# Performance work log

Measured on AMD Instinct MI355X. Metric: run time of the kernel, lower is better.

## Reference

```python
import jax, jax.numpy as jnp
import numpy as np
from jax import lax

DILATIONS = (1, 3, 9, 9, 3, 1)  # six mid blocks after the 1x1 input conv


def bilinear_sample(fm, verts):
    # fm: [B,H,W,C]; verts: [B,N,2] in [-1,1]; axis 0 of verts maps to H, axis 1 to W.
    # Matches jax.scipy.ndimage.map_coordinates(order=1, mode='constant'):
    # each out-of-bounds corner contributes 0.
    B, H, W, C = fm.shape
    scale = jnp.array([H - 1, W - 1], fm.dtype) / 2.0
    coords = (verts + 1.0) * scale  # [B,N,2]
    vy, vx = coords[..., 0], coords[..., 1]
    y0 = jnp.floor(vy)
    x0 = jnp.floor(vx)
    wy = (vy - y0)[..., None]
    wx = (vx - x0)[..., None]
    y0i = y0.astype(jnp.int32)
    x0i = x0.astype(jnp.int32)
    fm_flat = fm.reshape(B, H * W, C)

    def corner(yi, xi):
        valid = (yi >= 0) & (yi < H) & (xi >= 0) & (xi < W)
        idx = jnp.clip(yi, 0, H - 1) * W + jnp.clip(xi, 0, W - 1)  # [B,N]
        vals = jnp.take_along_axis(fm_flat, idx[..., None], axis=1)  # [B,N,C]
        return jnp.where(valid[..., None], vals, jnp.zeros((), fm.dtype))

    return ((1 - wy) * (1 - wx) * corner(y0i, x0i)
            + (1 - wy) * wx * corner(y0i, x0i + 1)
            + wy * (1 - wx) * corner(y0i + 1, x0i)
            + wy * wx * corner(y0i + 1, x0i + 1))


def conv1d(x, w, b, dil):
    # x: [B,N,Cin], w: [K,Cin,Cout]; flax nnx.Conv default: stride 1, SAME padding.
    out = lax.conv_general_dilated(x, w, (1,), 'SAME', rhs_dilation=(dil,),
                                   dimension_numbers=('NWC', 'WIO', 'NWC'))
    return out if b is None else out + b


def setup_inputs() -> dict:
    key = jax.random.key(0)
    ks = jax.random.split(key, 8)
    B, N, H, W, Cf, Ch = 16, 1024, 256, 256, 126, 512
    D = Cf + 2
    vertices = jax.random.uniform(ks[0], (B, N, 2), jnp.float32, -1.0, 1.0)
    feature_map = jax.random.normal(ks[1], (B, H, W, Cf), jnp.float32)
    w0 = jax.random.normal(ks[2], (1, D, Ch), jnp.float32) / np.float32(np.sqrt(D))
    b0 = jnp.zeros((Ch,), jnp.float32)
    ws = jax.random.normal(ks[3], (6, 3, Ch, Ch), jnp.float32) / np.float32(np.sqrt(3 * Ch))
    bs = jnp.zeros((6, Ch), jnp.float32)
    w_off = jax.random.normal(ks[4], (1, Ch, 2), jnp.float32) / np.float32(np.sqrt(Ch))
    return {"vertices": vertices, "feature_map": feature_map,
            "w0": w0, "b0": b0, "ws": ws, "bs": bs, "w_off": w_off}


def reference(vertices, feature_map, w0, b0, ws, bs, w_off):
    feat = bilinear_sample(feature_map, vertices)          # [B,N,Cf]
    x = jnp.concatenate([feat, vertices], axis=-1)         # [B,N,Cf+2]
    x = jax.nn.relu(conv1d(x, w0, b0, 1))                  # 1x1 input conv
    for i, dil in enumerate(DILATIONS):                    # fixed 6-layer stack
        x = jax.nn.relu(conv1d(x, ws[i], bs[i], dil))
    return conv1d(x, w_off, None, 1)                       # [B,N,2] offsets
```

## Files before the change

### kernel.cpp

```cpp
#include <hip/hip_runtime.h>

typedef __attribute__((ext_vector_type(4))) float f32x4;
typedef __attribute__((ext_vector_type(8))) _Float16 f16x8;

#define BM 128
#define BK 64

#define OFF_W0T 0
#define OFF_WT  131072
#define OFF_X0  (OFF_WT + 6*512*1536*2)
#define OFF_Y0  (OFF_X0 + 16384*128*2)
#define OFF_Y1  (OFF_Y0 + 16*1056*512*2)

__device__ __forceinline__ void load_lds16(const void* g, void* s) {
    __builtin_amdgcn_global_load_lds(
        (const __attribute__((address_space(1))) void*)g,
        (__attribute__((address_space(3))) void*)s, 16, 0, 0);
}

__global__ __launch_bounds__(256)
void wprep(const float* __restrict__ ws, const float* __restrict__ w0,
           _Float16* __restrict__ wt, _Float16* __restrict__ w0t)
{
    __shared__ float t[64][65];
    const int tid = threadIdx.x;
    const int tr = tid >> 6;
    const int tc = tid & 63;
    const int z = blockIdx.z;
    if (z < 18) {
        const int l = z / 3, tp = z % 3;
        const float* src = ws + (size_t)z * 512 * 512;
        const int ci0 = blockIdx.y * 64, co0 = blockIdx.x * 64;
        #pragma unroll
        for (int i = 0; i < 16; ++i) { int r = i*4 + tr; t[r][tc] = src[(ci0 + r)*512 + co0 + tc]; }
        __syncthreads();
        _Float16* dst = wt + (size_t)l * 512 * 1536;
        #pragma unroll
        for (int i = 0; i < 16; ++i) { int r = i*4 + tr; dst[(co0 + r)*1536 + tp*512 + ci0 + tc] = (_Float16)t[tc][r]; }
    } else {
        if (blockIdx.y >= 2) return;
        const int ci0 = blockIdx.y * 64, co0 = blockIdx.x * 64;
        #pragma unroll
        for (int i = 0; i < 16; ++i) { int r = i*4 + tr; t[r][tc] = w0[(ci0 + r)*512 + co0 + tc]; }
        __syncthreads();
        #pragma unroll
        for (int i = 0; i < 16; ++i) { int r = i*4 + tr; w0t[(co0 + r)*128 + ci0 + tc] = (_Float16)t[tc][r]; }
    }
}

__global__ __launch_bounds__(256)
void zeropad(_Float16* __restrict__ Y0, _Float16* __restrict__ Y1)
{
    const int i = blockIdx.x * 256 + threadIdx.x;
    const unsigned c2   = i & 255;
    const unsigned t2   = ((unsigned)i) >> 8;
    const unsigned prow = t2 & 31;
    const unsigned b    = (t2 >> 5) & 15;
    const unsigned buf  = t2 >> 9;
    const unsigned row  = prow < 16 ? prow : (1024 + prow);
    unsigned* p = (unsigned*)(buf ? Y1 : Y0);
    p[((size_t)b * 1056 + row) * 256 + c2] = 0u;
}

__global__ __launch_bounds__(256)
void sample_kernel(const float* __restrict__ verts, const float* __restrict__ fm,
                   _Float16* __restrict__ X0)
{
    const int p = blockIdx.x * 4 + (threadIdx.x >> 6);
    const int lane = threadIdx.x & 63;
    const int b = p >> 10;
    const float vy = verts[p*2], vx = verts[p*2 + 1];
    const float cy = (vy + 1.f) * 127.5f;
    const float cx = (vx + 1.f) * 127.5f;
    const float fy = floorf(cy), fx = floorf(cx);
    const int y0 = (int)fy, x0 = (int)fx;
    const float wy = cy - fy, wx = cx - fx;
    float w00 = (1.f - wy) * (1.f - wx), w01 = (1.f - wy) * wx;
    float w10 = wy * (1.f - wx),         w11 = wy * wx;
    const bool vy0 = (unsigned)y0 < 256u, vy1 = (unsigned)(y0 + 1) < 256u;
    const bool vx0 = (unsigned)x0 < 256u, vx1 = (unsigned)(x0 + 1) < 256u;
    w00 = (vy0 && vx0) ? w00 : 0.f;
    w01 = (vy0 && vx1) ? w01 : 0.f;
    w10 = (vy1 && vx0) ? w10 : 0.f;
    w11 = (vy1 && vx1) ? w11 : 0.f;
    const int yc0 = min(max(y0, 0), 255), yc1 = min(max(y0 + 1, 0), 255);
    const int xc0 = min(max(x0, 0), 255), xc1 = min(max(x0 + 1, 0), 255);
    const float* base = fm + (size_t)b * (256 * 256 * 126);
    const float* p00 = base + (yc0 * 256 + xc0) * 126;
    const float* p01 = base + (yc0 * 256 + xc1) * 126;
    const float* p10 = base + (yc1 * 256 + xc0) * 126;
    const float* p11 = base + (yc1 * 256 + xc1) * 126;
    _Float16* xr = X0 + (size_t)p * 128;
    for (int c = lane; c < 126; c += 64) {
        float a = w00 * p00[c] + w01 * p01[c] + w10 * p10[c] + w11 * p11[c];
        xr[c] = (_Float16)a;
    }
    if (lane < 2) xr[126 + lane] = (_Float16)(lane ? vx : vy);
}

template<int KTOT>
__global__ __launch_bounds__(256)
void conv_gemm(const _Float16* __restrict__ A, int a_row_stride, int a_batch_stride,
               const _Float16* __restrict__ WT, const float* __restrict__ bias,
               _Float16* __restrict__ Out, int o_row_stride, int o_batch_stride,
               int dil)
{
    __shared__ _Float16 Ald[BM * BK];
    __shared__ _Float16 Bld[BM * BK];
    const int tid  = threadIdx.x;
    const int wid  = tid >> 6;
    const int lane = tid & 63;
    const int b    = blockIdx.x >> 3;
    const int n0   = (blockIdx.x & 7) * BM;
    const int co0  = blockIdx.y * BM;
    const int wm   = wid >> 1, wn = wid & 1;

    const _Float16* Ab = A + (size_t)b * a_batch_stride + (size_t)n0 * a_row_stride;

    f32x4 acc[4][4] = {};

    const int srow = lane >> 3;
    const int scol = (lane & 7) * 8;

    for (int ks = 0; ks < KTOT / BK; ++ks) {
        int ci0, shift;
        if (KTOT == 128) { ci0 = ks * 64; shift = 0; }
        else             { int t = ks >> 3; ci0 = (ks & 7) * 64; shift = (t - 1) * dil; }
        const _Float16* Arow = Ab + (long)shift * a_row_stride + ci0 + scol;
        const _Float16* Brow = WT + (size_t)co0 * KTOT + ks * 64 + scol;
        #pragma unroll
        for (int i = 0; i < 4; ++i) {
            const int r0 = wid * 32 + i * 8;
            load_lds16(Arow + (size_t)(r0 + srow) * a_row_stride, &Ald[r0 * BK]);
            load_lds16(Brow + (size_t)(r0 + srow) * KTOT,         &Bld[r0 * BK]);
        }
        __syncthreads();
        #pragma unroll
        for (int kf = 0; kf < 2; ++kf) {
            f16x8 af[4], bfr[4];
            #pragma unroll
            for (int f = 0; f < 4; ++f) {
                af[f]  = *(const f16x8*)&Ald[(wm*64 + f*16 + (lane & 15)) * BK + kf*32 + (lane >> 4) * 8];
                bfr[f] = *(const f16x8*)&Bld[(wn*64 + f*16 + (lane & 15)) * BK + kf*32 + (lane >> 4) * 8];
            }
            #pragma unroll
            for (int m = 0; m < 4; ++m)
                #pragma unroll
                for (int n = 0; n < 4; ++n)
                    acc[m][n] = __builtin_amdgcn_mfma_f32_16x16x32_f16(af[m], bfr[n], acc[m][n], 0, 0, 0);
        }
        __syncthreads();
    }

    _Float16* Ob = Out + (size_t)b * o_batch_stride + (size_t)n0 * o_row_stride;
    #pragma unroll
    for (int n = 0; n < 4; ++n) {
        const int co = co0 + wn*64 + n*16 + (lane & 15);
        const float bv = bias[co];
        #pragma unroll
        for (int m = 0; m < 4; ++m) {
            #pragma unroll
            for (int j = 0; j < 4; ++j) {
                const int row = wm*64 + m*16 + (lane >> 4)*4 + j;
                float v = acc[m][n][j] + bv;
                v = fmaxf(v, 0.f);
                Ob[(size_t)row * o_row_stride + co] = (_Float16)v;
            }
        }
    }
}

#define NT8 24
__global__ __launch_bounds__(512, 2)
void conv_gemm8(const _Float16* __restrict__ A, const _Float16* __restrict__ WT,
                const float* __restrict__ bias, _Float16* __restrict__ Out, int dil)
{
    extern __shared__ _Float16 smem[];
    _Float16* Ald = smem;
    _Float16* Bld = smem + 3 * 256 * 64;

    const int tid  = threadIdx.x;
    const int wid  = tid >> 6;
    const int lane = tid & 63;
    const int wm   = wid >> 1;
    const int wn   = wid & 1;

    const int orig = blockIdx.x;
    const int swz  = (orig & 7) * 32 + (orig >> 3);
    const int nblk = swz & 3;
    const int mblk = swz >> 2;
    const int b     = mblk >> 2;
    const int n0row = (mblk & 3) * 256;
    const int co0   = nblk * 128;

    const _Float16* Ab = A + (size_t)b * (1056 * 512) + (size_t)n0row * 512;

    const int srow = lane >> 3;
    const int scol = (((lane & 7) ^ (lane >> 3)) << 3);

    f32x4 acc[4][4] = {};

    auto stageA = [&](int kt, int c, int ci0, int shift) {
        const int grow = 64 * c + 8 * wid + srow;
        const _Float16* src = Ab + (long)(grow + shift) * 512 + ci0 + scol;
        _Float16* dst = Ald + (kt % 3) * (256 * 64) + (64 * c + 8 * wid) * 64;
        load_lds16(src, dst);
    };
    auto stageB = [&](int kt, int c, int kk) {
        const int grow = 64 * c + 8 * wid + srow;
        const _Float16* src = WT + (size_t)(co0 + grow) * 1536 + kk + scol;
        _Float16* dst = Bld + (kt % 3) * (128 * 64) + (64 * c + 8 * wid) * 64;
        load_lds16(src, dst);
    };
    auto kinfo = [&](int ks, int& ci0, int& shift) {
        const int t = ks >> 3; ci0 = (ks & 7) * 64; shift = (t - 1) * dil;
    };

    {
        int ci0, sh;
        kinfo(0, ci0, sh);
        stageA(0, 0, ci0, sh); stageA(0, 1, ci0, sh); stageA(0, 2, ci0, sh); stageA(0, 3, ci0, sh);
        stageB(0, 0, 0); stageB(0, 1, 0);
        kinfo(1, ci0, sh);
        stageA(1, 0, ci0, sh); stageA(1, 1, ci0, sh); stageA(1, 2, ci0, sh); stageA(1, 3, ci0, sh);
        stageB(1, 0, 64); stageB(1, 1, 64);
    }

    #pragma unroll 1
    for (int kt = 0; kt < NT8; ++kt) {
        __builtin_amdgcn_sched_barrier(0);
        if (kt < NT8 - 1) asm volatile("s_waitcnt vmcnt(6)" ::: "memory");
        else              asm volatile("s_waitcnt vmcnt(0)" ::: "memory");
        __builtin_amdgcn_s_barrier();
        __builtin_amdgcn_sched_barrier(0);

        const _Float16* Abuf = Ald + (kt % 3) * (256 * 64);
        const _Float16* Bbuf = Bld + (kt % 3) * (128 * 64);
        const bool do_stage = (kt + 2 < NT8);
        int nci0 = 0, nsh = 0;
        if (do_stage) kinfo(kt + 2, nci0, nsh);

        f16x8 bfr[4][2], af[4][2];
        #pragma unroll
        for (int nf = 0; nf < 4; ++nf) {
            const int row = wn * 64 + nf * 16 + (lane & 15);
            #pragma unroll
            for (int kf = 0; kf < 2; ++kf) {
                const int slot = (kf * 4 + (lane >> 4)) ^ (row & 7);
                bfr[nf][kf] = *(const f16x8*)&Bbuf[row * 64 + slot * 8];
            }
        }
        {
            const int row = wm * 64 + 0 * 16 + (lane & 15);
            #pragma unroll
            for (int kf = 0; kf < 2; ++kf) {
                const int slot = (kf * 4 + (lane >> 4)) ^ (row & 7);
                af[0][kf] = *(const f16x8*)&Abuf[row * 64 + slot * 8];
            }
        }
        #pragma unroll
        for (int nf = 0; nf < 4; ++nf)
            #pragma unroll
            for (int kf = 0; kf < 2; ++kf)
                acc[0][nf] = __builtin_amdgcn_mfma_f32_16x16x32_f16(af[0][kf], bfr[nf][kf], acc[0][nf], 0, 0, 0);
        {
            const int row = wm * 64 + 1 * 16 + (lane & 15);
            #pragma unroll
            for (int kf = 0; kf < 2; ++kf) {
                const int slot = (kf * 4 + (lane >> 4)) ^ (row & 7);
                af[1][kf] = *(const f16x8*)&Abuf[row * 64 + slot * 8];
            }
        }
        if (do_stage) { stageA(kt + 2, 0, nci0, nsh); stageA(kt + 2, 1, nci0, nsh); stageA(kt + 2, 2, nci0, nsh); }
        #pragma unroll
        for (int nf = 0; nf < 4; ++nf)
            #pragma unroll
            for (int kf = 0; kf < 2; ++kf)
                acc[1][nf] = __builtin_amdgcn_mfma_f32_16x16x32_f16(af[1][kf], bfr[nf][kf], acc[1][nf], 0, 0, 0);
        {
            const int row = wm * 64 + 2 * 16 + (lane & 15);
            #pragma unroll
            for (int kf = 0; kf < 2; ++kf) {
                const int slot = (kf * 4 + (lane >> 4)) ^ (row & 7);
                af[2][kf] = *(const f16x8*)&Abuf[row * 64 + slot * 8];
            }
        }
        if (do_stage) { stageA(kt + 2, 3, nci0, nsh); stageB(kt + 2, 0, (kt + 2) * 64); stageB(kt + 2, 1, (kt + 2) * 64); }
        #pragma unroll
        for (int nf = 0; nf < 4; ++nf)
            #pragma unroll
            for (int kf = 0; kf < 2; ++kf)
                acc[2][nf] = __builtin_amdgcn_mfma_f32_16x16x32_f16(af[2][kf], bfr[nf][kf], acc[2][nf], 0, 0, 0);
        {
            const int row = wm * 64 + 3 * 16 + (lane & 15);
            #pragma unroll
            for (int kf = 0; kf < 2; ++kf) {
                const int slot = (kf * 4 + (lane >> 4)) ^ (row & 7);
                af[3][kf] = *(const f16x8*)&Abuf[row * 64 + slot * 8];
            }
        }
        #pragma unroll
        for (int nf = 0; nf < 4; ++nf)
            #pragma unroll
            for (int kf = 0; kf < 2; ++kf)
                acc[3][nf] = __builtin_amdgcn_mfma_f32_16x16x32_f16(af[3][kf], bfr[nf][kf], acc[3][nf], 0, 0, 0);

        __builtin_amdgcn_sched_group_barrier(0x100, 10, 0);
        __builtin_amdgcn_sched_group_barrier(0x008,  8, 0);
        __builtin_amdgcn_sched_group_barrier(0x100,  2, 0);
        __builtin_amdgcn_sched_group_barrier(0x070,  3, 0);
        __builtin_amdgcn_sched_group_barrier(0x008,  8, 0);
        __builtin_amdgcn_sched_group_barrier(0x100,  2, 0);
        __builtin_amdgcn_sched_group_barrier(0x070,  3, 0);
        __builtin_amdgcn_sched_group_barrier(0x008,  8, 0);
        __builtin_amdgcn_sched_group_barrier(0x100,  2, 0);
        __builtin_amdgcn_sched_group_barrier(0x008,  8, 0);
    }

    _Float16* Ob = Out + (size_t)b * (1056 * 512) + (size_t)n0row * 512;
    #pragma unroll
    for (int nf = 0; nf < 4; ++nf) {
        const int co = co0 + wn * 64 + nf * 16 + (lane & 15);
        const float bv = bias[co];
        #pragma unroll
        for (int m = 0; m < 4; ++m) {
            #pragma unroll
            for (int j = 0; j < 4; ++j) {
                const int row = wm * 64 + m * 16 + (lane >> 4) * 4 + j;
                float v = acc[m][nf][j] + bv;
                v = fmaxf(v, 0.f);
                Ob[(size_t)row * 512 + co] = (_Float16)v;
            }
        }
    }
}

__global__ __launch_bounds__(256)
void final_conv(const _Float16* __restrict__ Y, const float* __restrict__ woff,
                float* __restrict__ out)
{
    const int r = blockIdx.x * 4 + (threadIdx.x >> 6);
    const int lane = threadIdx.x & 63;
    const int b = r >> 10, n = r & 1023;
    const _Float16* yp = Y + ((size_t)b * 1056 + n) * 512 + lane * 8;
    f16x8 yv = *(const f16x8*)yp;
    const int ci0 = lane * 8;
    float s0 = 0.f, s1 = 0.f;
    #pragma unroll
    for (int e = 0; e < 8; ++e) {
        float y = (float)yv[e];
        s0 += y * woff[(ci0 + e) * 2 + 0];
        s1 += y * woff[(ci0 + e) * 2 + 1];
    }
    #pragma unroll
    for (int off = 32; off; off >>= 1) {
        s0 += __shfl_down(s0, off);
        s1 += __shfl_down(s1, off);
    }
    if (lane == 0) { out[r*2] = s0; out[r*2 + 1] = s1; }
}

extern "C" void kernel_launch(void* const* d_in, const int* in_sizes, int n_in,
                              void* d_out, int out_size, void* d_ws, size_t ws_size,
                              hipStream_t stream)
{
    const float* verts = (const float*)d_in[0];
    const float* fm    = (const float*)d_in[1];
    const float* w0    = (const float*)d_in[2];
    const float* b0    = (const float*)d_in[3];
    const float* ws    = (const float*)d_in[4];
    const float* bs    = (const float*)d_in[5];
    const float* woff  = (const float*)d_in[6];
    float* out = (float*)d_out;

    char* wsp = (char*)d_ws;
    _Float16* W0T = (_Float16*)(wsp + OFF_W0T);
    _Float16* WT  = (_Float16*)(wsp + OFF_WT);
    _Float16* X0  = (_Float16*)(wsp + OFF_X0);
    _Float16* Y0  = (_Float16*)(wsp + OFF_Y0);
    _Float16* Y1  = (_Float16*)(wsp + OFF_Y1);
    _Float16* Y0i = Y0 + 16 * 512;
    _Float16* Y1i = Y1 + 16 * 512;

    hipFuncSetAttribute(reinterpret_cast<const void*>(&conv_gemm8),
                        hipFuncAttributeMaxDynamicSharedMemorySize, 147456);

    wprep<<<dim3(8, 8, 19), 256, 0, stream>>>(ws, w0, WT, W0T);
    zeropad<<<1024, 256, 0, stream>>>(Y0, Y1);
    sample_kernel<<<4096, 256, 0, stream>>>(verts, fm, X0);

    conv_gemm<128><<<dim3(128, 4), 256, 0, stream>>>(
        X0, 128, 1024 * 128, W0T, b0, Y0i, 512, 1056 * 512, 1);

    const int DIL[6] = {1, 3, 9, 9, 3, 1};
    _Float16* bufs[2] = {Y0i, Y1i};
    for (int l = 0; l < 6; ++l) {
        conv_gemm8<<<256, 512, 147456, stream>>>(
            bufs[l & 1],
            WT + (size_t)l * 512 * 1536, bs + (size_t)l * 512,
            bufs[(l + 1) & 1], DIL[l]);
    }

    final_conv<<<4096, 256, 0, stream>>>(bufs[0], woff, out);
}
```

Baseline: 198.4 us.

## Reuse one A tile across all three conv taps with shifted LDS reads

The dilated-conv GEMM now stages a 320-row A chunk per 64-channel slice once and reads it three times with tap-dependent row shifts, instead of reloading a fresh 256-row A tile for every (tap, channel) k-step. The k-loop is restructured around channel chunks with compile-time tap specialisation, a double-buffered A halo tile, and three B buffers, each with its own wait counts and schedule groups. This cuts global and L2 traffic for A by roughly a factor of three and lowers dynamic LDS to 128 KB. In exchange the wait logic is more intricate and the swizzle key now depends on the shifted row, which risks bank conflicts or races if the counts are off. The halo assumes dil ≤ 32.

```diff
diff --git a/kernel.cpp b/kernel.cpp
--- a/kernel.cpp
+++ b/kernel.cpp
@@ -17,6 +17,8 @@
         (const __attribute__((address_space(1))) void*)g,
         (__attribute__((address_space(3))) void*)s, 16, 0, 0);
 }
+
+template<int N> struct IC { static constexpr int v = N; };
 
 __global__ __launch_bounds__(256)
 void wprep(const float* __restrict__ ws, const float* __restrict__ w0,
@@ -170,14 +172,15 @@
     }
 }
 
-#define NT8 24
+#define ACH_ELEMS (320 * 64)
+#define BBUF_ELEMS (128 * 64)
 __global__ __launch_bounds__(512, 2)
 void conv_gemm8(const _Float16* __restrict__ A, const _Float16* __restrict__ WT,
                 const float* __restrict__ bias, _Float16* __restrict__ Out, int dil)
 {
     extern __shared__ _Float16 smem[];
     _Float16* Ald = smem;
-    _Float16* Bld = smem + 3 * 256 * 64;
+    _Float16* Bld = smem + 2 * ACH_ELEMS;
 
     const int tid  = threadIdx.x;
     const int wid  = tid >> 6;
@@ -200,45 +203,38 @@
 
     f32x4 acc[4][4] = {};
 
-    auto stageA = [&](int kt, int c, int ci0, int shift) {
-        const int grow = 64 * c + 8 * wid + srow;
-        const _Float16* src = Ab + (long)(grow + shift) * 512 + ci0 + scol;
-        _Float16* dst = Ald + (kt % 3) * (256 * 64) + (64 * c + 8 * wid) * 64;
-        load_lds16(src, dst);
+    auto stageA1 = [&](int cn, int i) {
+        const int rb = 8 * (wid + 8 * i);
+        const _Float16* src = Ab + (long)(rb + srow - 32) * 512 + cn * 64 + scol;
+        load_lds16(src, Ald + (cn & 1) * ACH_ELEMS + rb * 64);
     };
-    auto stageB = [&](int kt, int c, int kk) {
-        const int grow = 64 * c + 8 * wid + srow;
-        const _Float16* src = WT + (size_t)(co0 + grow) * 1536 + kk + scol;
-        _Float16* dst = Bld + (kt % 3) * (128 * 64) + (64 * c + 8 * wid) * 64;
-        load_lds16(src, dst);
+    auto stageB1 = [&](int c2, int t2, int cc) {
+        const int grow = 64 * cc + 8 * wid + srow;
+        const _Float16* src = WT + (size_t)(co0 + grow) * 1536 + (t2 * 512 + c2 * 64) + scol;
+        load_lds16(src, Bld + t2 * BBUF_ELEMS + (64 * cc + 8 * wid) * 64);
     };
-    auto kinfo = [&](int ks, int& ci0, int& shift) {
-        const int t = ks >> 3; ci0 = (ks & 7) * 64; shift = (t - 1) * dil;
-    };
-
-    {
-        int ci0, sh;
-        kinfo(0, ci0, sh);
-        stageA(0, 0, ci0, sh); stageA(0, 1, ci0, sh); stageA(0, 2, ci0, sh); stageA(0, 3, ci0, sh);
-        stageB(0, 0, 0); stageB(0, 1, 0);
-        kinfo(1, ci0, sh);
-        stageA(1, 0, ci0, sh); stageA(1, 1, ci0, sh); stageA(1, 2, ci0, sh); stageA(1, 3, ci0, sh);
-        stageB(1, 0, 64); stageB(1, 1, 64);
-    }
-
-    #pragma unroll 1
-    for (int kt = 0; kt < NT8; ++kt) {
+
+    stageA1(0, 0); stageA1(0, 1); stageA1(0, 2); stageA1(0, 3); stageA1(0, 4);
+    stageB1(0, 0, 0); stageB1(0, 0, 1);
+    stageB1(0, 1, 0); stageB1(0, 1, 1);
+
+    auto body = [&](auto TAPc, auto DOAc, int c) {
+        constexpr int TAP = decltype(TAPc)::v;
+        constexpr int DOA = decltype(DOAc)::v;
+
         __builtin_amdgcn_sched_barrier(0);
-        if (kt < NT8 - 1) asm volatile("s_waitcnt vmcnt(6)" ::: "memory");
-        else              asm volatile("s_waitcnt vmcnt(0)" ::: "memory");
+        if constexpr (TAP == 1 && DOA)       asm volatile("s_waitcnt vmcnt(7)" ::: "memory");
+        else if constexpr (TAP == 2 && !DOA) asm volatile("s_waitcnt vmcnt(0)" ::: "memory");
+        else                                 asm volatile("s_waitcnt vmcnt(2)" ::: "memory");
         __builtin_amdgcn_s_barrier();
         __builtin_amdgcn_sched_barrier(0);
 
-        const _Float16* Abuf = Ald + (kt % 3) * (256 * 64);
-        const _Float16* Bbuf = Bld + (kt % 3) * (128 * 64);
-        const bool do_stage = (kt + 2 < NT8);
-        int nci0 = 0, nsh = 0;
-        if (do_stage) kinfo(kt + 2, nci0, nsh);
+        const _Float16* Abuf = Ald + (c & 1) * ACH_ELEMS;
+        const _Float16* Bbuf = Bld + TAP * BBUF_ELEMS;
+        const int shift = (TAP - 1) * dil;
+        const int rbase = 32 + wm * 64 + (lane & 15) + shift;
+        const int akey  = rbase & 7;
+        const int bkey  = lane & 7;
 
         f16x8 bfr[4][2], af[4][2];
         #pragma unroll
@@ -246,58 +242,61 @@
             const int row = wn * 64 + nf * 16 + (lane & 15);
             #pragma unroll
             for (int kf = 0; kf < 2; ++kf) {
-                const int slot = (kf * 4 + (lane >> 4)) ^ (row & 7);
+                const int slot = (kf * 4 + (lane >> 4)) ^ bkey;
                 bfr[nf][kf] = *(const f16x8*)&Bbuf[row * 64 + slot * 8];
             }
         }
-        {
-            const int row = wm * 64 + 0 * 16 + (lane & 15);
-            #pragma unroll
-            for (int kf = 0; kf < 2; ++kf) {
-                const int slot = (kf * 4 + (lane >> 4)) ^ (row & 7);
-                af[0][kf] = *(const f16x8*)&Abuf[row * 64 + slot * 8];
-            }
+        #pragma unroll
+        for (int kf = 0; kf < 2; ++kf) {
+            const int slot = (kf * 4 + (lane >> 4)) ^ akey;
+            af[0][kf] = *(const f16x8*)&Abuf[rbase * 64 + slot * 8];
         }
         #pragma unroll
         for (int nf = 0; nf < 4; ++nf)
             #pragma unroll
             for (int kf = 0; kf < 2; ++kf)
                 acc[0][nf] = __builtin_amdgcn_mfma_f32_16x16x32_f16(af[0][kf], bfr[nf][kf], acc[0][nf], 0, 0, 0);
-        {
-            const int row = wm * 64 + 1 * 16 + (lane & 15);
-            #pragma unroll
-            for (int kf = 0; kf < 2; ++kf) {
-                const int slot = (kf * 4 + (lane >> 4)) ^ (row & 7);
-                af[1][kf] = *(const f16x8*)&Abuf[row * 64 + slot * 8];
-            }
-        }
-        if (do_stage) { stageA(kt + 2, 0, nci0, nsh); stageA(kt + 2, 1, nci0, nsh); stageA(kt + 2, 2, nci0, nsh); }
+        #pragma unroll
+        for (int kf = 0; kf < 2; ++kf) {
+            const int slot = (kf * 4 + (lane >> 4)) ^ akey;
+            af[1][kf] = *(const f16x8*)&Abuf[(rbase + 16) * 64 + slot * 8];
+        }
+        if constexpr (TAP == 0 && DOA) {
+            stageA1(c + 1, 0); stageA1(c + 1, 1); stageA1(c + 1, 2); stageA1(c + 1, 3);
+        } else if constexpr (TAP == 0) {
+            stageB1(7, 2, 0);
+        } else if constexpr (DOA) {
+            if constexpr (TAP == 1) stageB1(c + 1, 0, 0);
+            else                    stageB1(c + 1, 1, 0);
+        }
         #pragma unroll
         for (int nf = 0; nf < 4; ++nf)
             #pragma unroll
             for (int kf = 0; kf < 2; ++kf)
                 acc[1][nf] = __builtin_amdgcn_mfma_f32_16x16x32_f16(af[1][kf], bfr[nf][kf], acc[1][nf], 0, 0, 0);
-        {
-            const int row = wm * 64 + 2 * 16 + (lane & 15);
-            #pragma unroll
-            for (int kf = 0; kf < 2; ++kf) {
-                const int slot = (kf * 4 + (lane >> 4)) ^ (row & 7);
-                af[2][kf] = *(const f16x8*)&Abuf[row * 64 + slot * 8];
-            }
-        }
-        if (do_stage) { stageA(kt + 2, 3, nci0, nsh); stageB(kt + 2, 0, (kt + 2) * 64); stageB(kt + 2, 1, (kt + 2) * 64); }
+        #pragma unroll
+        for (int kf = 0; kf < 2; ++kf) {
+            const int slot = (kf * 4 + (lane >> 4)) ^ akey;
+            af[2][kf] = *(const f16x8*)&Abuf[(rbase + 32) * 64 + slot * 8];
+        }
+        if constexpr (TAP == 0 && DOA) {
+            stageA1(c + 1, 4);
+            stageB1(c, 2, 0); stageB1(c, 2, 1);
+        } else if constexpr (TAP == 0) {
+            stageB1(7, 2, 1);
+        } else if constexpr (DOA) {
+            if constexpr (TAP == 1) stageB1(c + 1, 0, 1);
+            else                    stageB1(c + 1, 1, 1);
+        }
         #pragma unroll
         for (int nf = 0; nf < 4; ++nf)
             #pragma unroll
             for (int kf = 0; kf < 2; ++kf)
                 acc[2][nf] = __builtin_amdgcn_mfma_f32_16x16x32_f16(af[2][kf], bfr[nf][kf], acc[2][nf], 0, 0, 0);
-        {
-            const int row = wm * 64 + 3 * 16 + (lane & 15);
-            #pragma unroll
-            for (int kf = 0; kf < 2; ++kf) {
-                const int slot = (kf * 4 + (lane >> 4)) ^ (row & 7);
-                af[3][kf] = *(const f16x8*)&Abuf[row * 64 + slot * 8];
-            }
+        #pragma unroll
+        for (int kf = 0; kf < 2; ++kf) {
+            const int slot = (kf * 4 + (lane >> 4)) ^ akey;
+            af[3][kf] = *(const f16x8*)&Abuf[(rbase + 48) * 64 + slot * 8];
         }
         #pragma unroll
         for (int nf = 0; nf < 4; ++nf)
@@ -305,17 +304,42 @@
             for (int kf = 0; kf < 2; ++kf)
                 acc[3][nf] = __builtin_amdgcn_mfma_f32_16x16x32_f16(af[3][kf], bfr[nf][kf], acc[3][nf], 0, 0, 0);
 
-        __builtin_amdgcn_sched_group_barrier(0x100, 10, 0);
-        __builtin_amdgcn_sched_group_barrier(0x008,  8, 0);
-        __builtin_amdgcn_sched_group_barrier(0x100,  2, 0);
-        __builtin_amdgcn_sched_group_barrier(0x070,  3, 0);
-        __builtin_amdgcn_sched_group_barrier(0x008,  8, 0);
-        __builtin_amdgcn_sched_group_barrier(0x100,  2, 0);
-        __builtin_amdgcn_sched_group_barrier(0x070,  3, 0);
-        __builtin_amdgcn_sched_group_barrier(0x008,  8, 0);
-        __builtin_amdgcn_sched_group_barrier(0x100,  2, 0);
-        __builtin_amdgcn_sched_group_barrier(0x008,  8, 0);
-    }
+        if constexpr (DOA) {
+            if constexpr (TAP == 0) {
+                __builtin_amdgcn_sched_group_barrier(0x100, 10, 0);
+                __builtin_amdgcn_sched_group_barrier(0x008,  8, 0);
+                __builtin_amdgcn_sched_group_barrier(0x100,  2, 0);
+                __builtin_amdgcn_sched_group_barrier(0x070,  4, 0);
+                __builtin_amdgcn_sched_group_barrier(0x008,  8, 0);
+                __builtin_amdgcn_sched_group_barrier(0x100,  2, 0);
+                __builtin_amdgcn_sched_group_barrier(0x070,  3, 0);
+                __builtin_amdgcn_sched_group_barrier(0x008,  8, 0);
+                __builtin_amdgcn_sched_group_barrier(0x100,  2, 0);
+                __builtin_amdgcn_sched_group_barrier(0x008,  8, 0);
+            } else {
+                __builtin_amdgcn_sched_group_barrier(0x100, 10, 0);
+                __builtin_amdgcn_sched_group_barrier(0x008,  8, 0);
+                __builtin_amdgcn_sched_group_barrier(0x100,  2, 0);
+                __builtin_amdgcn_sched_group_barrier(0x070,  1, 0);
+                __builtin_amdgcn_sched_group_barrier(0x008,  8, 0);
+                __builtin_amdgcn_sched_group_barrier(0x100,  2, 0);
+                __builtin_amdgcn_sched_group_barrier(0x070,  1, 0);
+                __builtin_amdgcn_sched_group_barrier(0x008,  8, 0);
+                __builtin_amdgcn_sched_group_barrier(0x100,  2, 0);
+                __builtin_amdgcn_sched_group_barrier(0x008,  8, 0);
+            }
+        }
+    };
+
+    #pragma unroll 1
+    for (int c = 0; c < 7; ++c) {
+        body(IC<0>{}, IC<1>{}, c);
+        body(IC<1>{}, IC<1>{}, c);
+        body(IC<2>{}, IC<1>{}, c);
+    }
+    body(IC<0>{}, IC<0>{}, 7);
+    body(IC<1>{}, IC<0>{}, 7);
+    body(IC<2>{}, IC<0>{}, 7);
 
     _Float16* Ob = Out + (size_t)b * (1056 * 512) + (size_t)n0row * 512;
     #pragma unroll
@@ -383,7 +407,7 @@
     _Float16* Y1i = Y1 + 16 * 512;
 
     hipFuncSetAttribute(reinterpret_cast<const void*>(&conv_gemm8),
-                        hipFuncAttributeMaxDynamicSharedMemorySize, 147456);
+                        hipFuncAttributeMaxDynamicSharedMemorySize, 131072);
 
     wprep<<<dim3(8, 8, 19), 256, 0, stream>>>(ws, w0, WT, W0T);
     zeropad<<<1024, 256, 0, stream>>>(Y0, Y1);
@@ -395,7 +419,7 @@
     const int DIL[6] = {1, 3, 9, 9, 3, 1};
     _Float16* bufs[2] = {Y0i, Y1i};
     for (int l = 0; l < 6; ++l) {
-        conv_gemm8<<<256, 512, 147456, stream>>>(
+        conv_gemm8<<<256, 512, 131072, stream>>>(
             bufs[l & 1],
             WT + (size_t)l * 512 * 1536, bs + (size_t)l * 512,
             bufs[(l + 1) & 1], DIL[l]);
```

After: 179.3 us. -9.6%, faster.
